# Kernel optimization log

Measured on AMD Instinct MI355X. Metric: run time of the kernel, lower is better.

## Reference

```python
import jax, jax.numpy as jnp
import numpy as np

B, L, H, C = 2, 512, 128, 25

def setup_inputs() -> dict:
    key = jax.random.key(0)
    k1, k2, k3, k4 = jax.random.split(key, 4)
    x1 = jax.random.normal(k1, (B, L, H), dtype=jnp.float32)
    x2 = jax.random.normal(k2, (B, L, H), dtype=jnp.float32)
    W = jax.random.normal(k3, (C, 4 * H), dtype=jnp.float32) * (1.0 / np.sqrt(4 * H))
    b = jax.random.normal(k4, (C,), dtype=jnp.float32) * 0.01
    return {"x1": x1, "x2": x2, "W": W, "b": b}

def reference(x1, x2, W, b):
    # feat = cat([x1_i, x2_j, x1_i*x2_j, |x1_i - x2_j|]) over all (i, j) pairs,
    # then Linear(4H -> C). Split W into its 4 H-sized blocks so we never
    # materialize the [B, L, L, 4H] concatenated tensor.
    Hd = x1.shape[-1]
    W1, W2, W3, W4 = (W[:, 0:Hd], W[:, Hd:2*Hd], W[:, 2*Hd:3*Hd], W[:, 3*Hd:4*Hd])
    a = x1[:, :, None, :]   # [B, L, 1, H] -> row token
    c = x2[:, None, :, :]   # [B, 1, L, H] -> col token
    # a@W1 and c@W2 depend on only one index, so compute [B, L, C] then broadcast.
    t1 = jnp.einsum('blh,ch->blc', x1, W1)[:, :, None, :]  # [B, L, 1, C]
    t2 = jnp.einsum('blh,ch->blc', x2, W2)[:, None, :, :]  # [B, 1, L, C]
    # product term is a bilinear contraction; no [B,L,L,H] materialization needed.
    t3 = jnp.einsum('blh,bmh,ch->blmc', x1, x2, W3)         # [B, L, L, C]
    # abs-diff term requires the pairwise [B, L, L, H] tensor (nonlinear in pair).
    t4 = jnp.einsum('blmh,ch->blmc', jnp.abs(a - c), W4)    # [B, L, L, C]
    return t1 + t2 + t3 + t4 + b  # [B, L, L, C]
```

## Files before the change

kernel.cpp:

```cpp
#include <hip/hip_runtime.h>
#include <hip/hip_bf16.h>
#include <math.h>

#define BB 2
#define LL 512
#define HH 128
#define CC 25
#define W4H (4*HH)

typedef __attribute__((ext_vector_type(4))) float    f32x4;
typedef __attribute__((ext_vector_type(8))) _Float16 half8;
typedef __attribute__((ext_vector_type(2))) _Float16 half2t;
typedef __attribute__((ext_vector_type(4))) unsigned uint4v;

#define T1_OFF 0
#define T2_OFF (BB*LL*CC)
#define WFT_BYTE_OFF (2*BB*LL*CC*4)

#define MTILE 64
#define LPB   8
#define XPH   136

static __device__ __forceinline__ half8 habs8(half8 x) {
    uint4v u = __builtin_bit_cast(uint4v, x);
    u &= 0x7FFF7FFFu;
    return __builtin_bit_cast(half8, u);
}

static __device__ __forceinline__ half2t pkrtz(float a, float b) {
    return __builtin_bit_cast(half2t, __builtin_amdgcn_cvt_pkrtz(a, b));
}

union H4 { half2t h2[2]; unsigned long long u64; };

__global__ __launch_bounds__(256)
void prep_kernel(const float* __restrict__ x1, const float* __restrict__ x2,
                 const float* __restrict__ W, const float* __restrict__ bias,
                 float* __restrict__ ws)
{
    const int tid = threadIdx.x;
    const int c   = blockIdx.y;
    const int bl  = blockIdx.x * 256 + tid;

    if (blockIdx.y == 0) {
        _Float16* wft = (_Float16*)((char*)ws + WFT_BYTE_OFF);
        for (int idx = blockIdx.x * 256 + tid; idx < 32 * 256; idx += 4 * 256) {
            const int cc = idx >> 8;
            const int k  = idx & 255;
            float v = 0.f;
            if (cc < CC) v = (k < HH) ? W[(size_t)cc * W4H + 2*HH + k]
                                      : W[(size_t)cc * W4H + 3*HH + (k - HH)];
            wft[idx] = (_Float16)v;
        }
    }

    const float* w1  = W + (size_t)c * W4H;
    const float* w2  = w1 + HH;
    const float* xr1 = x1 + (size_t)bl * HH;
    const float* xr2 = x2 + (size_t)bl * HH;

    float s1a = 0.f, s1b = 0.f, s2a = 0.f, s2b = 0.f;
    #pragma unroll
    for (int i = 0; i < 32; i += 2) {
        const f32x4 a0 = *(const f32x4*)(xr1 + i*4);
        const f32x4 a1 = *(const f32x4*)(xr1 + i*4 + 4);
        const f32x4 b0 = *(const f32x4*)(xr2 + i*4);
        const f32x4 b1 = *(const f32x4*)(xr2 + i*4 + 4);
        const f32x4 u0 = *(const f32x4*)(w1 + i*4);
        const f32x4 u1 = *(const f32x4*)(w1 + i*4 + 4);
        const f32x4 v0 = *(const f32x4*)(w2 + i*4);
        const f32x4 v1 = *(const f32x4*)(w2 + i*4 + 4);
        #pragma unroll
        for (int j = 0; j < 4; ++j) {
            s1a = fmaf(a0[j], u0[j], s1a);
            s1b = fmaf(a1[j], u1[j], s1b);
            s2a = fmaf(b0[j], v0[j], s2a);
            s2b = fmaf(b1[j], v1[j], s2b);
        }
    }
    ws[T1_OFF + bl * CC + c] = s1a + s1b + bias[c];
    ws[T2_OFF + bl * CC + c] = s2a + s2b;
}

__global__ __launch_bounds__(256)
void biaffine_mfma(const float* __restrict__ x1, const float* __restrict__ x2,
                   const float* __restrict__ ws, float* __restrict__ out)
{
    __shared__ __align__(16) _Float16 x2h[MTILE * XPH];
    __shared__ __align__(16) _Float16 x1h[LPB * XPH];

    const int tid = threadIdx.x;
    const int b   = blockIdx.z;
    const int l0  = blockIdx.y * LPB;
    const int m0  = blockIdx.x * MTILE;

    const int lane = tid & 63;
    const int wv   = tid >> 6;
    const int q    = lane >> 4;
    const int cn   = lane & 15;

    const _Float16* wft = (const _Float16*)((const char*)ws + WFT_BYTE_OFF);
    half8 Bf[2][8];
    #pragma unroll
    for (int t = 0; t < 2; ++t)
        #pragma unroll
        for (int kk = 0; kk < 8; ++kk)
            Bf[t][kk] = *(const half8*)(wft + ((cn + 16*t) * 256 + kk * 32 + q * 8));

    {
        const float* sx2 = x2 + ((size_t)b * LL + m0) * HH;
        #pragma unroll
        for (int i = 0; i < 8; ++i) {
            const int idx = i * 256 + tid;
            const int r   = idx >> 5;
            const int c4  = idx & 31;
            const f32x4 v = *(const f32x4*)(sx2 + r * HH + c4 * 4);
            H4 h;
            h.h2[0] = pkrtz(v[0], v[1]);
            h.h2[1] = pkrtz(v[2], v[3]);
            *(unsigned long long*)(&x2h[r * XPH + c4 * 4]) = h.u64;
        }
        const float* sx1 = x1 + ((size_t)b * LL + l0) * HH;
        const int r  = tid >> 5;
        const int c4 = tid & 31;
        const f32x4 v = *(const f32x4*)(sx1 + r * HH + c4 * 4);
        H4 h;
        h.h2[0] = pkrtz(v[0], v[1]);
        h.h2[1] = pkrtz(v[2], v[3]);
        *(unsigned long long*)(&x1h[r * XPH + c4 * 4]) = h.u64;
    }
    __syncthreads();

    const int mrowA = wv * 16 + cn;
    half8 X2f[4];
    #pragma unroll
    for (int hh = 0; hh < 4; ++hh)
        X2f[hh] = *(const half8*)(&x2h[mrowA * XPH + hh * 32 + q * 8]);

    const float* Tb1 = ws + T1_OFF;
    const float* Tb2 = ws + T2_OFF;
    float t2a[4], t2b[4];
    #pragma unroll
    for (int r = 0; r < 4; ++r) {
        const int mg = m0 + wv * 16 + q * 4 + r;
        t2a[r] = Tb2[((size_t)b * LL + mg) * CC + cn];
        t2b[r] = (cn + 16 < CC) ? Tb2[((size_t)b * LL + mg) * CC + cn + 16] : 0.f;
    }

    #pragma unroll
    for (int l = 0; l < LPB; ++l) {
        const int lg = l0 + l;
        const float t1a = Tb1[((size_t)b * LL + lg) * CC + cn];
        const float t1b = (cn + 16 < CC) ? Tb1[((size_t)b * LL + lg) * CC + cn + 16] : 0.f;

        f32x4 acc0 = {0.f, 0.f, 0.f, 0.f};
        f32x4 acc1 = {0.f, 0.f, 0.f, 0.f};

        #pragma unroll
        for (int hh = 0; hh < 4; ++hh) {
            const half8 a  = *(const half8*)(&x1h[l * XPH + hh * 32 + q * 8]);
            const half8 bq = X2f[hh];
            const half8 Ap = a * bq;
            const half8 Ad = habs8(a - bq);
            acc0 = __builtin_amdgcn_mfma_f32_16x16x32_f16(Ap, Bf[0][hh],     acc0, 0, 0, 0);
            acc1 = __builtin_amdgcn_mfma_f32_16x16x32_f16(Ap, Bf[1][hh],     acc1, 0, 0, 0);
            acc0 = __builtin_amdgcn_mfma_f32_16x16x32_f16(Ad, Bf[0][hh + 4], acc0, 0, 0, 0);
            acc1 = __builtin_amdgcn_mfma_f32_16x16x32_f16(Ad, Bf[1][hh + 4], acc1, 0, 0, 0);
        }

        #pragma unroll
        for (int r = 0; r < 4; ++r) {
            const int mg = m0 + wv * 16 + q * 4 + r;
            float* o = out + (((size_t)b * LL + lg) * LL + mg) * CC;
            o[cn] = acc0[r] + t1a + t2a[r];
            if (cn + 16 < CC) o[cn + 16] = acc1[r] + t1b + t2b[r];
        }
    }
}

extern "C" void kernel_launch(void* const* d_in, const int* in_sizes, int n_in,
                              void* d_out, int out_size, void* d_ws, size_t ws_size,
                              hipStream_t stream) {
    const float* x1   = (const float*)d_in[0];
    const float* x2   = (const float*)d_in[1];
    const float* W    = (const float*)d_in[2];
    const float* bias = (const float*)d_in[3];
    float* out = (float*)d_out;
    float* ws  = (float*)d_ws;

    dim3 pgrid(BB * LL / 256, CC);
    prep_kernel<<<pgrid, 256, 0, stream>>>(x1, x2, W, bias, ws);

    dim3 grid(LL / MTILE, LL / LPB, BB);
    biaffine_mfma<<<grid, 256, 0, stream>>>(x1, x2, ws, out);
}
```

Before: 102.2 us.

## Fuse prep kernel into main MFMA kernel, folding t1/t2 into extra MFMAs

Drops the separate prep kernel. Each block now converts W to fp16 MFMA fragments in shared memory itself, and the x1@W1 and x2@W2 terms are computed as four extra MFMAs per K-chunk rather than being precomputed and read back from workspace. This removes one kernel launch and the workspace round trip. In exchange, every block redoes the W conversion (32KB of shared memory), MFMA work per output doubles, and many more registers are held (32 half8 B fragments). The t1/t2 terms also drop from fp32 FMA to fp16 inputs.

Result: faster. 92.33 us (-9.7%).

```diff
diff --git a/kernel.cpp b/kernel.cpp
--- a/kernel.cpp
+++ b/kernel.cpp
@@ -13,10 +13,6 @@
 typedef __attribute__((ext_vector_type(2))) _Float16 half2t;
 typedef __attribute__((ext_vector_type(4))) unsigned uint4v;
 
-#define T1_OFF 0
-#define T2_OFF (BB*LL*CC)
-#define WFT_BYTE_OFF (2*BB*LL*CC*4)
-
 #define MTILE 64
 #define LPB   8
 #define XPH   136
@@ -26,66 +22,18 @@
     u &= 0x7FFF7FFFu;
     return __builtin_bit_cast(half8, u);
 }
-
 static __device__ __forceinline__ half2t pkrtz(float a, float b) {
     return __builtin_bit_cast(half2t, __builtin_amdgcn_cvt_pkrtz(a, b));
 }
-
 union H4 { half2t h2[2]; unsigned long long u64; };
+union H8 { half2t h2[4]; uint4v u4; half8 h8; };
 
 __global__ __launch_bounds__(256)
-void prep_kernel(const float* __restrict__ x1, const float* __restrict__ x2,
-                 const float* __restrict__ W, const float* __restrict__ bias,
-                 float* __restrict__ ws)
+void biaffine_fused(const float* __restrict__ x1, const float* __restrict__ x2,
+                    const float* __restrict__ W, const float* __restrict__ bias,
+                    float* __restrict__ out)
 {
-    const int tid = threadIdx.x;
-    const int c   = blockIdx.y;
-    const int bl  = blockIdx.x * 256 + tid;
-
-    if (blockIdx.y == 0) {
-        _Float16* wft = (_Float16*)((char*)ws + WFT_BYTE_OFF);
-        for (int idx = blockIdx.x * 256 + tid; idx < 32 * 256; idx += 4 * 256) {
-            const int cc = idx >> 8;
-            const int k  = idx & 255;
-            float v = 0.f;
-            if (cc < CC) v = (k < HH) ? W[(size_t)cc * W4H + 2*HH + k]
-                                      : W[(size_t)cc * W4H + 3*HH + (k - HH)];
-            wft[idx] = (_Float16)v;
-        }
-    }
-
-    const float* w1  = W + (size_t)c * W4H;
-    const float* w2  = w1 + HH;
-    const float* xr1 = x1 + (size_t)bl * HH;
-    const float* xr2 = x2 + (size_t)bl * HH;
-
-    float s1a = 0.f, s1b = 0.f, s2a = 0.f, s2b = 0.f;
-    #pragma unroll
-    for (int i = 0; i < 32; i += 2) {
-        const f32x4 a0 = *(const f32x4*)(xr1 + i*4);
-        const f32x4 a1 = *(const f32x4*)(xr1 + i*4 + 4);
-        const f32x4 b0 = *(const f32x4*)(xr2 + i*4);
-        const f32x4 b1 = *(const f32x4*)(xr2 + i*4 + 4);
-        const f32x4 u0 = *(const f32x4*)(w1 + i*4);
-        const f32x4 u1 = *(const f32x4*)(w1 + i*4 + 4);
-        const f32x4 v0 = *(const f32x4*)(w2 + i*4);
-        const f32x4 v1 = *(const f32x4*)(w2 + i*4 + 4);
-        #pragma unroll
-        for (int j = 0; j < 4; ++j) {
-            s1a = fmaf(a0[j], u0[j], s1a);
-            s1b = fmaf(a1[j], u1[j], s1b);
-            s2a = fmaf(b0[j], v0[j], s2a);
-            s2b = fmaf(b1[j], v1[j], s2b);
-        }
-    }
-    ws[T1_OFF + bl * CC + c] = s1a + s1b + bias[c];
-    ws[T2_OFF + bl * CC + c] = s2a + s2b;
-}
-
-__global__ __launch_bounds__(256)
-void biaffine_mfma(const float* __restrict__ x1, const float* __restrict__ x2,
-                   const float* __restrict__ ws, float* __restrict__ out)
-{
+    __shared__ __align__(16) _Float16 wfrag[2048 * 8];
     __shared__ __align__(16) _Float16 x2h[MTILE * XPH];
     __shared__ __align__(16) _Float16 x1h[LPB * XPH];
 
@@ -99,13 +47,26 @@
     const int q    = lane >> 4;
     const int cn   = lane & 15;
 
-    const _Float16* wft = (const _Float16*)((const char*)ws + WFT_BYTE_OFF);
-    half8 Bf[2][8];
     #pragma unroll
-    for (int t = 0; t < 2; ++t)
-        #pragma unroll
-        for (int kk = 0; kk < 8; ++kk)
-            Bf[t][kk] = *(const half8*)(wft + ((cn + 16*t) * 256 + kk * 32 + q * 8));
+    for (int i = 0; i < 8; ++i) {
+        const int fid = i * 256 + tid;
+        const int ln  = fid & 63;
+        const int t   = (fid >> 6) & 1;
+        const int kk  = fid >> 7;
+        const int c   = (ln & 15) + 16 * t;
+        const int k0  = kk * 32 + ((ln >> 4) << 3);
+        const int wc  = (k0 + 256) & 511;
+        H8 h; h.u4 = (uint4v){0u, 0u, 0u, 0u};
+        if (c < CC) {
+            const f32x4 v0 = *(const f32x4*)(W + (size_t)c * W4H + wc);
+            const f32x4 v1 = *(const f32x4*)(W + (size_t)c * W4H + wc + 4);
+            h.h2[0] = pkrtz(v0[0], v0[1]);
+            h.h2[1] = pkrtz(v0[2], v0[3]);
+            h.h2[2] = pkrtz(v1[0], v1[1]);
+            h.h2[3] = pkrtz(v1[2], v1[3]);
+        }
+        *(uint4v*)(&wfrag[fid * 8]) = h.u4;
+    }
 
     {
         const float* sx2 = x2 + ((size_t)b * LL + m0) * HH;
@@ -131,28 +92,24 @@
     }
     __syncthreads();
 
+    half8 Bf0[16], Bf1[16];
+    #pragma unroll
+    for (int kk = 0; kk < 16; ++kk) {
+        Bf0[kk] = *(const half8*)(&wfrag[((kk * 2 + 0) * 64 + lane) * 8]);
+        Bf1[kk] = *(const half8*)(&wfrag[((kk * 2 + 1) * 64 + lane) * 8]);
+    }
+
     const int mrowA = wv * 16 + cn;
     half8 X2f[4];
     #pragma unroll
     for (int hh = 0; hh < 4; ++hh)
         X2f[hh] = *(const half8*)(&x2h[mrowA * XPH + hh * 32 + q * 8]);
 
-    const float* Tb1 = ws + T1_OFF;
-    const float* Tb2 = ws + T2_OFF;
-    float t2a[4], t2b[4];
-    #pragma unroll
-    for (int r = 0; r < 4; ++r) {
-        const int mg = m0 + wv * 16 + q * 4 + r;
-        t2a[r] = Tb2[((size_t)b * LL + mg) * CC + cn];
-        t2b[r] = (cn + 16 < CC) ? Tb2[((size_t)b * LL + mg) * CC + cn + 16] : 0.f;
-    }
+    const float ba = bias[cn];
+    const float bb = (cn + 16 < CC) ? bias[cn + 16] : 0.f;
 
     #pragma unroll
     for (int l = 0; l < LPB; ++l) {
-        const int lg = l0 + l;
-        const float t1a = Tb1[((size_t)b * LL + lg) * CC + cn];
-        const float t1b = (cn + 16 < CC) ? Tb1[((size_t)b * LL + lg) * CC + cn + 16] : 0.f;
-
         f32x4 acc0 = {0.f, 0.f, 0.f, 0.f};
         f32x4 acc1 = {0.f, 0.f, 0.f, 0.f};
 
@@ -162,18 +119,23 @@
             const half8 bq = X2f[hh];
             const half8 Ap = a * bq;
             const half8 Ad = habs8(a - bq);
-            acc0 = __builtin_amdgcn_mfma_f32_16x16x32_f16(Ap, Bf[0][hh],     acc0, 0, 0, 0);
-            acc1 = __builtin_amdgcn_mfma_f32_16x16x32_f16(Ap, Bf[1][hh],     acc1, 0, 0, 0);
-            acc0 = __builtin_amdgcn_mfma_f32_16x16x32_f16(Ad, Bf[0][hh + 4], acc0, 0, 0, 0);
-            acc1 = __builtin_amdgcn_mfma_f32_16x16x32_f16(Ad, Bf[1][hh + 4], acc1, 0, 0, 0);
+            acc0 = __builtin_amdgcn_mfma_f32_16x16x32_f16(Ap, Bf0[hh],      acc0, 0, 0, 0);
+            acc1 = __builtin_amdgcn_mfma_f32_16x16x32_f16(Ap, Bf1[hh],      acc1, 0, 0, 0);
+            acc0 = __builtin_amdgcn_mfma_f32_16x16x32_f16(Ad, Bf0[4 + hh],  acc0, 0, 0, 0);
+            acc1 = __builtin_amdgcn_mfma_f32_16x16x32_f16(Ad, Bf1[4 + hh],  acc1, 0, 0, 0);
+            acc0 = __builtin_amdgcn_mfma_f32_16x16x32_f16(a,  Bf0[8 + hh],  acc0, 0, 0, 0);
+            acc1 = __builtin_amdgcn_mfma_f32_16x16x32_f16(a,  Bf1[8 + hh],  acc1, 0, 0, 0);
+            acc0 = __builtin_amdgcn_mfma_f32_16x16x32_f16(bq, Bf0[12 + hh], acc0, 0, 0, 0);
+            acc1 = __builtin_amdgcn_mfma_f32_16x16x32_f16(bq, Bf1[12 + hh], acc1, 0, 0, 0);
         }
 
+        const int lg = l0 + l;
         #pragma unroll
         for (int r = 0; r < 4; ++r) {
             const int mg = m0 + wv * 16 + q * 4 + r;
             float* o = out + (((size_t)b * LL + lg) * LL + mg) * CC;
-            o[cn] = acc0[r] + t1a + t2a[r];
-            if (cn + 16 < CC) o[cn + 16] = acc1[r] + t1b + t2b[r];
+            o[cn] = acc0[r] + ba;
+            if (cn + 16 < CC) o[cn + 16] = acc1[r] + bb;
         }
     }
 }
@@ -186,11 +148,7 @@
     const float* W    = (const float*)d_in[2];
     const float* bias = (const float*)d_in[3];
     float* out = (float*)d_out;
-    float* ws  = (float*)d_ws;
-
-    dim3 pgrid(BB * LL / 256, CC);
-    prep_kernel<<<pgrid, 256, 0, stream>>>(x1, x2, W, bias, ws);
 
     dim3 grid(LL / MTILE, LL / LPB, BB);
-    biaffine_mfma<<<grid, 256, 0, stream>>>(x1, x2, ws, out);
+    biaffine_fused<<<grid, 256, 0, stream>>>(x1, x2, W, bias, out);
 }
```
